# Optimization experiments

Hardware: AMD Instinct MI355X
Metric: run time of the kernel (lower is better)

## Reference

```python
import jax, jax.numpy as jnp
import numpy as np

TAU = 3.0          # CPG tau
VTH = 1.0          # LIF v_threshold (v_reset = 0, hard reset)
PEAK = 16          # peak population size
NUM_E = 25         # int(32 * 0.8) excitatory neurons
FATIGUE_TH = 8
ALPHA = 4.0        # spikingjelly sigmoid surrogate alpha (unused in fwd)


def spike_fn(x):
    # Heaviside threshold at 0 (v >= VTH fires)
    return (x >= 0.0).astype(x.dtype)


def setup_inputs() -> dict:
    key = jax.random.key(0)
    k0, k1, k2, k3, k4 = jax.random.split(key, 5)
    B, N = 524288, 32
    spike_history = (jax.random.uniform(k0, (B, N)) < 0.3).astype(jnp.float32)
    neighbor_E_spikes = (jax.random.uniform(k1, (B, 8, NUM_E)) < 0.3).astype(jnp.float32)
    # mutual_inhibition: -2.0 everywhere, within-population blocks *0.1 -> -0.2,
    # cross-population blocks set to -3.0
    is_peak = jnp.arange(N) < PEAK
    same_pop = is_peak[:, None] == is_peak[None, :]
    mutual_inhibition = jnp.where(same_pop, -0.2, -3.0).astype(jnp.float32)
    coupling_W = jax.random.normal(k2, (N, NUM_E), dtype=jnp.float32) * 0.2
    peak_fatigue = jax.random.randint(k3, (B,), 0, 10, dtype=jnp.int32)
    trough_fatigue = jax.random.randint(k4, (B,), 0, 10, dtype=jnp.int32)
    v0 = jnp.zeros((B, N), dtype=jnp.float32)
    return {
        "spike_history": spike_history,
        "neighbor_E_spikes": neighbor_E_spikes,
        "mutual_inhibition": mutual_inhibition,
        "coupling_W": coupling_W,
        "v0": v0,
        "peak_fatigue": peak_fatigue,
        "trough_fatigue": trough_fatigue,
        "num_ticks": 5,
    }


def reference(spike_history, neighbor_E_spikes, mutual_inhibition, coupling_W,
              v0, peak_fatigue, trough_fatigue, num_ticks):
    B = spike_history.shape[0]
    # fatigue-driven drive: trough fatigue excites peak half, peak fatigue excites trough half
    dp = jnp.where(trough_fatigue >= FATIGUE_TH, 2.0, 0.0)[:, None]  # [B,1]
    dt = jnp.where(peak_fatigue >= FATIGUE_TH, 2.0, 0.0)[:, None]
    drive = jnp.concatenate(
        [jnp.broadcast_to(dp, (B, PEAK)), jnp.broadcast_to(dt, (B, 32 - PEAK))], axis=-1)
    # neighbor coupling: sum_k W @ nbr_k ; constant across ticks, hoisted out of loop
    coupling = jnp.einsum('bkn,mn->bm', neighbor_E_spikes, coupling_W)
    base = drive + 0.3 * coupling  # [B,32]

    def step(carry, _):
        v, sh, acc = carry
        recurrent = jnp.einsum('bn,mn->bm', sh, mutual_inhibition)  # sh @ M.T
        x = base + 0.5 * recurrent
        # LIF (decay_input=True): v += (x - (v - v_reset)) / tau, v_reset = 0
        v = v + (x - v) / TAU
        s = spike_fn(v - VTH)
        v = v * (1.0 - s)  # hard reset to 0
        return (v, s, acc + s), None

    init = (v0, spike_history, jnp.zeros_like(v0))
    (v, sh, acc), _ = jax.lax.scan(step, init, None, length=num_ticks)
    should_stay = acc[:, PEAK:].sum(axis=-1) > 0.5  # trough active => STAY
    return acc[:, :NUM_E], should_stay
```

## Files before the change

kernel.cpp:

```cpp
#include <hip/hip_runtime.h>


#define FATIGUE_TH 8

__global__ __launch_bounds__(256) void AgentLSM_70841190580507_kernel(
    const float* __restrict__ sh_in,
    const float* __restrict__ nbr,
    const float* __restrict__ M,
    const float* __restrict__ W,
    const int*   __restrict__ pf,
    const int*   __restrict__ tf,
    const int*   __restrict__ ticks_p,
    float* __restrict__ out_acc,
    float* __restrict__ out_stay,
    int B)
{
    __shared__ float4 lds_nbr4[400];
    __shared__ float4 lds_W4[200];
    __shared__ float  lds_cnt[8 * 33];
    __shared__ float  lds_out[200];
    __shared__ float  lds_stay[8];

    float* lds_nbr = (float*)lds_nbr4;
    float* lds_W   = (float*)lds_W4;

    const int tid = threadIdx.x;
    const int g   = tid >> 5;
    const int m   = tid & 31;
    const long long b = (long long)blockIdx.x * 8 + g;
    const bool valid = (b < (long long)B);
    const int nv = min(8, B - blockIdx.x * 8);

    if (tid < 200) lds_W4[tid] = ((const float4*)W)[tid];

    {
        const long long fbase = (long long)blockIdx.x * 1600;
        const long long ftot  = (long long)B * 200;
        const float4* nb4 = (const float4*)nbr;
        #pragma unroll
        for (int i = tid; i < 400; i += 256) {
            long long f0 = fbase + (long long)i * 4;
            lds_nbr4[i] = (f0 + 3 < ftot) ? nb4[fbase / 4 + i]
                                          : make_float4(0.f, 0.f, 0.f, 0.f);
        }
    }
    __syncthreads();

    if (m < 25) {
        float c = 0.f;
        #pragma unroll
        for (int k = 0; k < 8; ++k) c += lds_nbr[g * 200 + k * 25 + m];
        lds_cnt[g * 33 + m] = c;
    }
    __syncthreads();

    float coup = 0.f;
    #pragma unroll
    for (int n = 0; n < 25; ++n)
        coup += lds_cnt[g * 33 + n] * lds_W[m * 25 + n];

    const float a_same  = M[0];
    const float a_cross = M[16];

    float drive = 0.f;
    int init_bit = 0;
    if (valid) {
        drive = (m < 16) ? ((tf[b] >= FATIGUE_TH) ? 2.0f : 0.0f)
                         : ((pf[b] >= FATIGUE_TH) ? 2.0f : 0.0f);
        init_bit = (sh_in[b * 32 + m] != 0.0f);
    }
    float base = drive + 0.3f * coup;
    float v = 0.0f;

    unsigned long long bal = __ballot(init_bit);
    unsigned int mask = (unsigned int)(bal >> (tid & 32));

    const int T = ticks_p[0];
    int acc = 0;
    unsigned int any_tr = 0;
    const bool is_peak = (m < 16);

    #define TICK()  do {                                                   \
        float Spf = (float)__popc(mask & 0xFFFFu);                         \
        float Stf = (float)__popc(mask >> 16);                             \
        float rec = is_peak ? (a_same * Spf + a_cross * Stf)               \
                            : (a_cross * Spf + a_same * Stf);              \
        float x = base + 0.5f * rec;                                       \
        v = v + (x - v) / 3.0f;                  \
        bool s = (v >= 1.0f);                 \
        unsigned long long sb = __ballot(s);                               \
        mask = (unsigned int)(sb >> (tid & 32));                           \
        any_tr |= (mask >> 16);                                            \
        acc += s ? 1 : 0;                                                  \
        v = s ? 0.0f : v;                                                  \
    } while (0)

    if (T == 5) {
        TICK(); TICK(); TICK(); TICK(); TICK();
    } else {
        for (int t = 0; t < T; ++t) TICK();
    }
    #undef TICK

    if (m < 25) lds_out[g * 25 + m] = (float)acc;
    if (m == 31) lds_stay[g] = any_tr ? 1.0f : 0.0f;
    __syncthreads();

    const long long obase = (long long)blockIdx.x * 200;
    if (nv == 8) {
        if (tid < 50)
            ((float4*)out_acc)[obase / 4 + tid] =
                ((const float4*)lds_out)[tid];
        if (tid < 8)
            out_stay[(long long)blockIdx.x * 8 + tid] = lds_stay[tid];
    } else {
        if (tid < nv * 25) out_acc[obase + tid] = lds_out[tid];
        if (tid < nv)      out_stay[(long long)blockIdx.x * 8 + tid] = lds_stay[tid];
    }
}

extern "C" void kernel_launch(void* const* d_in, const int* in_sizes, int n_in,
                              void* d_out, int out_size, void* d_ws, size_t ws_size,
                              hipStream_t stream) {
    const float* sh    = (const float*)d_in[0];
    const float* nbr   = (const float*)d_in[1];
    const float* M     = (const float*)d_in[2];
    const float* W     = (const float*)d_in[3];
    const int*   pf    = (const int*)d_in[5];
    const int*   tf    = (const int*)d_in[6];
    const int*   ticks = (const int*)d_in[7];

    const int B = in_sizes[5];
    float* out_acc  = (float*)d_out;
    float* out_stay = out_acc + (long long)B * 25;

    const int blocks = (B + 7) / 8;
    AgentLSM_70841190580507_kernel<<<blocks, 256, 0, stream>>>(
        sh, nbr, M, W, pf, tf, ticks, out_acc, out_stay, B);
}
```

Measured before the change: 640.5 us.

## Make each wavefront stage its own neighbor rows to drop block barriers

Each 64-lane wavefront now loads the neighbor-spike rows for its own two agents into LDS and writes its own output slice. This removes three of the four block-wide __syncthreads; only the barrier after the shared W load remains. The output store changes from float4 writes by one wave to per-wave scalar writes with bounds checks. It relies on intra-wavefront lockstep for LDS visibility between the load and reduction phases, which is fragile but fine on AMD wave64.

```diff
diff --git a/kernel.cpp b/kernel.cpp
--- a/kernel.cpp
+++ b/kernel.cpp
@@ -15,52 +15,35 @@
     float* __restrict__ out_stay,
     int B)
 {
+    __shared__ float4 lds_W4[200];
     __shared__ float4 lds_nbr4[400];
-    __shared__ float4 lds_W4[200];
-    __shared__ float  lds_cnt[8 * 33];
+    __shared__ float  lds_cnt[8 * 26];
     __shared__ float  lds_out[200];
     __shared__ float  lds_stay[8];
 
-    float* lds_nbr = (float*)lds_nbr4;
-    float* lds_W   = (float*)lds_W4;
-
     const int tid = threadIdx.x;
+    const int w   = tid >> 6;
+    const int l   = tid & 63;
     const int g   = tid >> 5;
     const int m   = tid & 31;
     const long long b = (long long)blockIdx.x * 8 + g;
     const bool valid = (b < (long long)B);
-    const int nv = min(8, B - blockIdx.x * 8);
 
     if (tid < 200) lds_W4[tid] = ((const float4*)W)[tid];
+    __syncthreads();
 
+    const float4* nb4 = (const float4*)nbr;
+    const long long cbase = (long long)blockIdx.x * 400 + w * 100;
+    const long long ctot  = (long long)B * 50;
+    const float4 z = make_float4(0.f, 0.f, 0.f, 0.f);
     {
-        const long long fbase = (long long)blockIdx.x * 1600;
-        const long long ftot  = (long long)B * 200;
-        const float4* nb4 = (const float4*)nbr;
-        #pragma unroll
-        for (int i = tid; i < 400; i += 256) {
-            long long f0 = fbase + (long long)i * 4;
-            lds_nbr4[i] = (f0 + 3 < ftot) ? nb4[fbase / 4 + i]
-                                          : make_float4(0.f, 0.f, 0.f, 0.f);
+        long long c0 = cbase + l;
+        lds_nbr4[w * 100 + l] = (c0 < ctot) ? nb4[c0] : z;
+        if (l < 36) {
+            long long c1 = cbase + 64 + l;
+            lds_nbr4[w * 100 + 64 + l] = (c1 < ctot) ? nb4[c1] : z;
         }
     }
-    __syncthreads();
-
-    if (m < 25) {
-        float c = 0.f;
-        #pragma unroll
-        for (int k = 0; k < 8; ++k) c += lds_nbr[g * 200 + k * 25 + m];
-        lds_cnt[g * 33 + m] = c;
-    }
-    __syncthreads();
-
-    float coup = 0.f;
-    #pragma unroll
-    for (int n = 0; n < 25; ++n)
-        coup += lds_cnt[g * 33 + n] * lds_W[m * 25 + n];
-
-    const float a_same  = M[0];
-    const float a_cross = M[16];
 
     float drive = 0.f;
     int init_bit = 0;
@@ -69,13 +52,30 @@
                          : ((pf[b] >= FATIGUE_TH) ? 2.0f : 0.0f);
         init_bit = (sh_in[b * 32 + m] != 0.0f);
     }
+    const float a_same  = M[0];
+    const float a_cross = M[16];
+    const int T = ticks_p[0];
+
+    const float* lds_nbr = (const float*)lds_nbr4;
+    if (m < 25) {
+        float c = 0.f;
+        #pragma unroll
+        for (int k = 0; k < 8; ++k) c += lds_nbr[g * 200 + k * 25 + m];
+        lds_cnt[g * 26 + m] = c;
+    }
+
+    const float* lds_W = (const float*)lds_W4;
+    float coup = 0.f;
+    #pragma unroll
+    for (int n = 0; n < 25; ++n)
+        coup += lds_cnt[g * 26 + n] * lds_W[m * 25 + n];
+
     float base = drive + 0.3f * coup;
     float v = 0.0f;
 
     unsigned long long bal = __ballot(init_bit);
     unsigned int mask = (unsigned int)(bal >> (tid & 32));
 
-    const int T = ticks_p[0];
     int acc = 0;
     unsigned int any_tr = 0;
     const bool is_peak = (m < 16);
@@ -104,18 +104,14 @@
 
     if (m < 25) lds_out[g * 25 + m] = (float)acc;
     if (m == 31) lds_stay[g] = any_tr ? 1.0f : 0.0f;
-    __syncthreads();
 
-    const long long obase = (long long)blockIdx.x * 200;
-    if (nv == 8) {
-        if (tid < 50)
-            ((float4*)out_acc)[obase / 4 + tid] =
-                ((const float4*)lds_out)[tid];
-        if (tid < 8)
-            out_stay[(long long)blockIdx.x * 8 + tid] = lds_stay[tid];
-    } else {
-        if (tid < nv * 25) out_acc[obase + tid] = lds_out[tid];
-        if (tid < nv)      out_stay[(long long)blockIdx.x * 8 + tid] = lds_stay[tid];
+    const long long obase = (long long)blockIdx.x * 200 + w * 50;
+    if (l < 50) {
+        long long o = obase + l;
+        if (o < (long long)B * 25) out_acc[o] = lds_out[w * 50 + l];
+    } else if (l < 52) {
+        long long sbi = (long long)blockIdx.x * 8 + w * 2 + (l - 50);
+        if (sbi < (long long)B) out_stay[sbi] = lds_stay[w * 2 + (l - 50)];
     }
 }
 
```

After: 657.5 us. 2.7% more time.
